# Performance work log

Hardware: AMD Instinct MI355X
Metric: run time of the kernel (lower is better)

The kernel has to match this reference:

```python
import jax, jax.numpy as jnp
import numpy as np


def setup_inputs() -> dict:
    key = jax.random.key(0)
    k1, k2, k3, k4 = jax.random.split(key, 4)
    B, Sq, Sk, d = 16, 2048, 2048, 64
    queries = jax.random.normal(k1, (B, Sq, d), dtype=jnp.float32)
    keys = jax.random.normal(k2, (B, Sk, d), dtype=jnp.float32)
    values = jax.random.normal(k3, (B, Sk, d), dtype=jnp.float32)
    # True = padded key position (masked out)
    key_padding_mask = jax.random.randint(k4, (B, Sk), 0, 2) == 1
    return {"queries": queries, "keys": keys, "values": values,
            "key_padding_mask": key_padding_mask}


def reference(queries, keys, values, key_padding_mask):
    d = queries.shape[-1]
    # scores: [B, Sq, Sk]
    scores = jnp.einsum("bqd,bkd->bqk", queries, keys) / jnp.sqrt(
        jnp.asarray(d, dtype=queries.dtype))
    # padded keys get -inf before softmax (mask broadcast over query dim)
    scores = jnp.where(key_padding_mask[:, None, :], -jnp.inf, scores)
    attention_weights = jax.nn.softmax(scores, axis=2)
    return jnp.einsum("bqk,bkd->bqd", attention_weights, values)
```

## Files before the change

kernel.cpp:

```cpp
#include <hip/hip_runtime.h>
#include <hip/hip_bf16.h>

#define NB 16
#define SQ 2048
#define SK 2048
#define DH 64
#define RS 72
#define NKT (SK / 64)

#define KBLK 1024
#define VBLK 512
#define BBLK 128

typedef __attribute__((ext_vector_type(8))) short short8;
typedef __attribute__((ext_vector_type(8))) __bf16 bf16x8;
typedef __attribute__((ext_vector_type(4))) float floatx4;
typedef __attribute__((ext_vector_type(2))) unsigned uint2v;

__device__ __forceinline__ unsigned pk2(float a, float b) {
  __hip_bfloat162 h = __float22bfloat162_rn(make_float2(a, b));
  unsigned u; __builtin_memcpy(&u, &h, 4); return u;
}
__device__ __forceinline__ short bf1(float a) {
  __hip_bfloat16 h = __float2bfloat16(a);
  short s; __builtin_memcpy(&s, &h, 2); return s;
}
__device__ __forceinline__ floatx4 mfma16(short8 a, short8 b, floatx4 c) {
  return __builtin_amdgcn_mfma_f32_16x16x32_bf16(
      __builtin_bit_cast(bf16x8, a), __builtin_bit_cast(bf16x8, b), c, 0, 0, 0);
}

__global__ __launch_bounds__(256)
void prepass(const float* __restrict__ K, const float* __restrict__ V,
             const int* __restrict__ m, short* __restrict__ Kb,
             short* __restrict__ Vt, float* __restrict__ bias) {
  __shared__ short tl[64 * RS];
  const int blk = blockIdx.x;
  const int t = threadIdx.x;
  if (blk < KBLK) {
    size_t i8 = ((size_t)blk * 256 + t) * 8;
    floatx4 a = *(const floatx4*)(K + i8);
    floatx4 b = *(const floatx4*)(K + i8 + 4);
    union { unsigned u[4]; short8 s; } w;
    w.u[0] = pk2(a[0], a[1]); w.u[1] = pk2(a[2], a[3]);
    w.u[2] = pk2(b[0], b[1]); w.u[3] = pk2(b[2], b[3]);
    *(short8*)(Kb + i8) = w.s;
  } else if (blk < KBLK + VBLK) {
    const int bt = blk - KBLK;
    const int key = t >> 2, d0 = (t & 3) * 16;
    const float* src = V + ((size_t)bt * 64 + key) * 64 + d0;
#pragma unroll
    for (int c = 0; c < 4; ++c) {
      floatx4 v = *(const floatx4*)(src + 4 * c);
#pragma unroll
      for (int j = 0; j < 4; ++j) tl[(d0 + 4 * c + j) * RS + key] = bf1(v[j]);
    }
    __syncthreads();
    short* dst = Vt + (size_t)bt * 4096;
#pragma unroll
    for (int i = 0; i < 2; ++i) {
      int idx = i * 2048 + t * 8;
      int row = idx >> 6, col = idx & 63;
      *(short8*)(dst + idx) = *(const short8*)(tl + row * RS + col);
    }
  } else {
    int i = (blk - KBLK - VBLK) * 256 + t;
    bias[i] = m[i] ? -1e30f : 0.0f;
  }
}

__global__ __launch_bounds__(256)
void attn_main(const float* __restrict__ Q, const short* __restrict__ Kb,
               const short* __restrict__ Vt, const float* __restrict__ bias,
               float* __restrict__ Out) {
  __shared__ __align__(16) short ks[64 * RS];
  __shared__ __align__(16) short vt[64 * RS];
  __shared__ __align__(16) short pb[4 * 16 * RS];

  const int b    = blockIdx.x >> 5;
  const int qt   = blockIdx.x & 31;
  const int tid  = threadIdx.x;
  const int wave = tid >> 6;
  const int lane = tid & 63;
  const int L    = lane & 15;
  const int quad = lane >> 4;
  const int q0w  = qt * 64 + wave * 16;

  const float QS = 0.125f * 1.4426950408889634f;
  short8 qf[2];
  {
    const float* qp = Q + ((size_t)b * SQ + q0w + L) * DH + 8 * quad;
#pragma unroll
    for (int c = 0; c < 2; ++c) {
      floatx4 a  = *(const floatx4*)(qp + 32 * c);
      floatx4 a2 = *(const floatx4*)(qp + 32 * c + 4);
      union { unsigned u[4]; short8 s; } w;
      w.u[0] = pk2(a[0] * QS, a[1] * QS);
      w.u[1] = pk2(a[2] * QS, a[3] * QS);
      w.u[2] = pk2(a2[0] * QS, a2[1] * QS);
      w.u[3] = pk2(a2[2] * QS, a2[3] * QS);
      qf[c] = w.s;
    }
  }

  floatx4 o[4];
#pragma unroll
  for (int n = 0; n < 4; ++n) o[n] = (floatx4){0.f, 0.f, 0.f, 0.f};
  float m_q = -1e30f, l_q = 0.f;

  short* pbw = pb + wave * 16 * RS;

  const short* kg = Kb + (size_t)b * SK * DH;
  const short* vg = Vt + (size_t)b * 32 * 4096;
  const float* bg = bias + b * SK;

  const int srow = tid >> 3;
  const int scol = (tid & 7) * 8;

  short8 kr[2], vr[2];
#pragma unroll
  for (int i = 0; i < 2; ++i) {
    kr[i] = *(const short8*)(kg + i * 2048 + tid * 8);
    vr[i] = *(const short8*)(vg + i * 2048 + tid * 8);
  }

  for (int kt = 0; kt < NKT; ++kt) {
#pragma unroll
    for (int i = 0; i < 2; ++i) {
      int row = i * 32 + srow;
      *(short8*)(ks + row * RS + scol) = kr[i];
      *(short8*)(vt + row * RS + scol) = vr[i];
    }
    __syncthreads();

    if (kt + 1 < NKT) {
      const short* kn = kg + (size_t)(kt + 1) * 4096;
      const short* vn = vg + (size_t)(kt + 1) * 4096;
#pragma unroll
      for (int i = 0; i < 2; ++i) {
        kr[i] = *(const short8*)(kn + i * 2048 + tid * 8);
        vr[i] = *(const short8*)(vn + i * 2048 + tid * 8);
      }
    }

    floatx4 s[4];
#pragma unroll
    for (int t = 0; t < 4; ++t) {
      short8 kf0 = *(short8*)(ks + (16 * t + L) * RS + quad * 8);
      short8 kf1 = *(short8*)(ks + (16 * t + L) * RS + 32 + quad * 8);
      floatx4 z = (floatx4){0.f, 0.f, 0.f, 0.f};
      s[t] = mfma16(kf0, qf[0], z);
      s[t] = mfma16(kf1, qf[1], s[t]);
    }

    const float* bq = bg + kt * 64 + 4 * quad;
    float a[4][4];
    float rm = -1e30f;
#pragma unroll
    for (int t = 0; t < 4; ++t) {
      floatx4 bv = *(const floatx4*)(bq + 16 * t);
#pragma unroll
      for (int r = 0; r < 4; ++r) {
        a[t][r] = s[t][r] + bv[r];
        rm = fmaxf(rm, a[t][r]);
      }
    }
    rm = fmaxf(rm, __shfl_xor(rm, 16));
    rm = fmaxf(rm, __shfl_xor(rm, 32));
    float mn = fmaxf(m_q, rm);
    float alpha_q = __builtin_amdgcn_exp2f(m_q - mn);
    m_q = mn;

    float rs = 0.f;
#pragma unroll
    for (int t = 0; t < 4; ++t) {
      float p0 = __builtin_amdgcn_exp2f(a[t][0] - mn);
      float p1 = __builtin_amdgcn_exp2f(a[t][1] - mn);
      float p2 = __builtin_amdgcn_exp2f(a[t][2] - mn);
      float p3 = __builtin_amdgcn_exp2f(a[t][3] - mn);
      rs += (p0 + p1) + (p2 + p3);
      uint2v w; w.x = pk2(p0, p1); w.y = pk2(p2, p3);
      *(uint2v*)(pbw + L * RS + 16 * t + 4 * quad) = w;
    }
    rs += __shfl_xor(rs, 16);
    rs += __shfl_xor(rs, 32);
    l_q = alpha_q * l_q + rs;

    float av[4];
#pragma unroll
    for (int r = 0; r < 4; ++r) av[r] = __shfl(alpha_q, quad * 4 + r);
#pragma unroll
    for (int n = 0; n < 4; ++n)
#pragma unroll
      for (int r = 0; r < 4; ++r) o[n][r] *= av[r];

    short8 pf0 = *(short8*)(pbw + L * RS + quad * 8);
    short8 pf1 = *(short8*)(pbw + L * RS + 32 + quad * 8);

#pragma unroll
    for (int n = 0; n < 4; ++n) {
      short8 vf0 = *(short8*)(vt + (16 * n + L) * RS + quad * 8);
      short8 vf1 = *(short8*)(vt + (16 * n + L) * RS + 32 + quad * 8);
      o[n] = mfma16(pf0, vf0, o[n]);
      o[n] = mfma16(pf1, vf1, o[n]);
    }
    __syncthreads();
  }

#pragma unroll
  for (int r = 0; r < 4; ++r) {
    float lv = __shfl(l_q, quad * 4 + r);
    float inv = 1.0f / lv;
    size_t row = (size_t)b * SQ + q0w + quad * 4 + r;
#pragma unroll
    for (int n = 0; n < 4; ++n)
      Out[row * DH + 16 * n + L] = o[n][r] * inv;
  }
}

extern "C" void kernel_launch(void* const* d_in, const int* in_sizes, int n_in,
                              void* d_out, int out_size, void* d_ws, size_t ws_size,
                              hipStream_t stream) {
  const float* Q = (const float*)d_in[0];
  const float* K = (const float*)d_in[1];
  const float* V = (const float*)d_in[2];
  const int* mask = (const int*)d_in[3];
  float* Out = (float*)d_out;

  short* Kb   = (short*)d_ws;
  short* Vt   = (short*)((char*)d_ws + (size_t)NB * SK * DH * 2);
  float* bias = (float*)((char*)d_ws + (size_t)NB * SK * DH * 4);

  prepass  <<<KBLK + VBLK + BBLK, 256, 0, stream>>>(K, V, mask, Kb, Vt, bias);
  attn_main<<<NB * (SQ / 64), 256, 0, stream>>>(Q, Kb, Vt, bias, Out);
}
```

Before: 121.2 us.

## Split key dimension across two blocks and merge partial softmax in a combine kernel

Splits the key sequence into two halves processed by separate blocks, doubling the grid from 512 to 1024 workgroups. Each half writes its unnormalized output plus the running max and sum, and a new combine kernel rescales and merges the two partials. This is meant to fill more of the GPU's compute units and hide latency, at the cost of an extra kernel launch and extra global traffic for the partial outputs. The V transpose prepass is also reworked to pack two keys per 32-bit shared store, cutting shared-memory store count and bank conflicts.

```diff
diff --git a/kernel.cpp b/kernel.cpp
--- a/kernel.cpp
+++ b/kernel.cpp
@@ -21,10 +21,6 @@
   __hip_bfloat162 h = __float22bfloat162_rn(make_float2(a, b));
   unsigned u; __builtin_memcpy(&u, &h, 4); return u;
 }
-__device__ __forceinline__ short bf1(float a) {
-  __hip_bfloat16 h = __float2bfloat16(a);
-  short s; __builtin_memcpy(&s, &h, 2); return s;
-}
 __device__ __forceinline__ floatx4 mfma16(short8 a, short8 b, floatx4 c) {
   return __builtin_amdgcn_mfma_f32_16x16x32_bf16(
       __builtin_bit_cast(bf16x8, a), __builtin_bit_cast(bf16x8, b), c, 0, 0, 0);
@@ -34,7 +30,7 @@
 void prepass(const float* __restrict__ K, const float* __restrict__ V,
              const int* __restrict__ m, short* __restrict__ Kb,
              short* __restrict__ Vt, float* __restrict__ bias) {
-  __shared__ short tl[64 * RS];
+  __shared__ unsigned tlw[64 * 33];
   const int blk = blockIdx.x;
   const int t = threadIdx.x;
   if (blk < KBLK) {
@@ -47,21 +43,27 @@
     *(short8*)(Kb + i8) = w.s;
   } else if (blk < KBLK + VBLK) {
     const int bt = blk - KBLK;
-    const int key = t >> 2, d0 = (t & 3) * 16;
-    const float* src = V + ((size_t)bt * 64 + key) * 64 + d0;
-#pragma unroll
-    for (int c = 0; c < 4; ++c) {
-      floatx4 v = *(const floatx4*)(src + 4 * c);
-#pragma unroll
-      for (int j = 0; j < 4; ++j) tl[(d0 + 4 * c + j) * RS + key] = bf1(v[j]);
+    const int key2 = t & 31;
+    const int dg = (t >> 5) * 8;
+    const float* vp0 = V + ((size_t)bt * 64 + 2 * key2) * 64 + dg;
+    const float* vp1 = vp0 + 64;
+    floatx4 va  = *(const floatx4*)(vp0);
+    floatx4 va2 = *(const floatx4*)(vp0 + 4);
+    floatx4 vb  = *(const floatx4*)(vp1);
+    floatx4 vb2 = *(const floatx4*)(vp1 + 4);
+#pragma unroll
+    for (int j = 0; j < 4; ++j) {
+      tlw[(dg + j) * 33 + key2]     = pk2(va[j],  vb[j]);
+      tlw[(dg + 4 + j) * 33 + key2] = pk2(va2[j], vb2[j]);
     }
     __syncthreads();
+    const short* tls = (const short*)tlw;
     short* dst = Vt + (size_t)bt * 4096;
 #pragma unroll
     for (int i = 0; i < 2; ++i) {
       int idx = i * 2048 + t * 8;
-      int row = idx >> 6, col = idx & 63;
-      *(short8*)(dst + idx) = *(const short8*)(tl + row * RS + col);
+      int d = idx >> 6, key = idx & 63;
+      *(short8*)(dst + idx) = *(const short8*)(tls + d * 66 + key);
     }
   } else {
     int i = (blk - KBLK - VBLK) * 256 + t;
@@ -72,19 +74,23 @@
 __global__ __launch_bounds__(256)
 void attn_main(const float* __restrict__ Q, const short* __restrict__ Kb,
                const short* __restrict__ Vt, const float* __restrict__ bias,
-               float* __restrict__ Out) {
+               float* __restrict__ Out, float* __restrict__ Op1,
+               float2* __restrict__ ml) {
   __shared__ __align__(16) short ks[64 * RS];
   __shared__ __align__(16) short vt[64 * RS];
   __shared__ __align__(16) short pb[4 * 16 * RS];
 
-  const int b    = blockIdx.x >> 5;
-  const int qt   = blockIdx.x & 31;
+  const int half = blockIdx.x >> 9;
+  const int rest = blockIdx.x & 511;
+  const int b    = rest >> 5;
+  const int qt   = rest & 31;
   const int tid  = threadIdx.x;
+  const int lane = tid & 63;
   const int wave = tid >> 6;
-  const int lane = tid & 63;
   const int L    = lane & 15;
   const int quad = lane >> 4;
   const int q0w  = qt * 64 + wave * 16;
+  const int kt0  = half << 4;
 
   const float QS = 0.125f * 1.4426950408889634f;
   short8 qf[2];
@@ -120,11 +126,11 @@
   short8 kr[2], vr[2];
 #pragma unroll
   for (int i = 0; i < 2; ++i) {
-    kr[i] = *(const short8*)(kg + i * 2048 + tid * 8);
-    vr[i] = *(const short8*)(vg + i * 2048 + tid * 8);
-  }
-
-  for (int kt = 0; kt < NKT; ++kt) {
+    kr[i] = *(const short8*)(kg + (size_t)kt0 * 4096 + i * 2048 + tid * 8);
+    vr[i] = *(const short8*)(vg + (size_t)kt0 * 4096 + i * 2048 + tid * 8);
+  }
+
+  for (int kt = kt0; kt < kt0 + 16; ++kt) {
 #pragma unroll
     for (int i = 0; i < 2; ++i) {
       int row = i * 32 + srow;
@@ -133,7 +139,7 @@
     }
     __syncthreads();
 
-    if (kt + 1 < NKT) {
+    if (kt + 1 < kt0 + 16) {
       const short* kn = kg + (size_t)(kt + 1) * 4096;
       const short* vn = vg + (size_t)(kt + 1) * 4096;
 #pragma unroll
@@ -207,15 +213,40 @@
     __syncthreads();
   }
 
+  float* Od = half ? Op1 : Out;
 #pragma unroll
   for (int r = 0; r < 4; ++r) {
-    float lv = __shfl(l_q, quad * 4 + r);
-    float inv = 1.0f / lv;
     size_t row = (size_t)b * SQ + q0w + quad * 4 + r;
 #pragma unroll
     for (int n = 0; n < 4; ++n)
-      Out[row * DH + 16 * n + L] = o[n][r] * inv;
-  }
+      Od[row * DH + 16 * n + L] = o[n][r];
+  }
+  if (lane < 16)
+    ml[((size_t)half * NB + b) * SQ + q0w + lane] = make_float2(m_q, l_q);
+}
+
+__global__ __launch_bounds__(256)
+void combine(const float* __restrict__ Op1, const float2* __restrict__ ml,
+             float* __restrict__ Out) {
+  int idx = blockIdx.x * 256 + threadIdx.x;
+  int q = idx >> 3;
+  int dc = (idx & 7) * 8;
+  float2 s0 = ml[q];
+  float2 s1 = ml[NB * SQ + q];
+  float M = fmaxf(s0.x, s1.x);
+  float w0 = __builtin_amdgcn_exp2f(s0.x - M);
+  float w1 = __builtin_amdgcn_exp2f(s1.x - M);
+  float inv = 1.0f / (s0.y * w0 + s1.y * w1);
+  const float* p0 = Out + (size_t)q * DH + dc;
+  const float* p1 = Op1 + (size_t)q * DH + dc;
+  floatx4 a0 = *(const floatx4*)(p0);
+  floatx4 a1 = *(const floatx4*)(p0 + 4);
+  floatx4 b0 = *(const floatx4*)(p1);
+  floatx4 b1 = *(const floatx4*)(p1 + 4);
+  floatx4 r0 = (a0 * w0 + b0 * w1) * inv;
+  floatx4 r1 = (a1 * w0 + b1 * w1) * inv;
+  *(floatx4*)(Out + (size_t)q * DH + dc) = r0;
+  *(floatx4*)(Out + (size_t)q * DH + dc + 4) = r1;
 }
 
 extern "C" void kernel_launch(void* const* d_in, const int* in_sizes, int n_in,
@@ -227,10 +258,14 @@
   const int* mask = (const int*)d_in[3];
   float* Out = (float*)d_out;
 
-  short* Kb   = (short*)d_ws;
-  short* Vt   = (short*)((char*)d_ws + (size_t)NB * SK * DH * 2);
-  float* bias = (float*)((char*)d_ws + (size_t)NB * SK * DH * 4);
+  char* ws = (char*)d_ws;
+  short*  Kb   = (short*)(ws);
+  short*  Vt   = (short*)(ws + 4194304);
+  float*  bias = (float*)(ws + 8388608);
+  float2* ml   = (float2*)(ws + 8519680);
+  float*  Op1  = (float*)(ws + 9043968);
 
   prepass  <<<KBLK + VBLK + BBLK, 256, 0, stream>>>(K, V, mask, Kb, Vt, bias);
-  attn_main<<<NB * (SQ / 64), 256, 0, stream>>>(Q, Kb, Vt, bias, Out);
-}
+  attn_main<<<2 * NB * (SQ / 64), 256, 0, stream>>>(Q, Kb, Vt, bias, Out, Op1, ml);
+  combine  <<<NB * SQ * DH / 8 / 256, 256, 0, stream>>>(Op1, ml, Out);
+}
```

After: 126.1 us. +4.0%, slower.
